# Performance work log

Hardware: AMD Instinct MI355X
Metric: run time of the kernel (lower is better)

## Reference

```python
import jax, jax.numpy as jnp
import numpy as np

N_HEAD = 16  # matches init_kwargs


def _rope_cos_sin(T, head_dim):
    # inv_freq over even indices, as in AdvancedRotaryEmbedding
    inv_freq = 1.0 / (10000.0 ** (jnp.arange(0, head_dim, 2, dtype=jnp.float32) / head_dim))
    t = jnp.arange(T, dtype=jnp.float32)
    freqs = t[:, None] * inv_freq[None, :]  # [T, head_dim/2]
    return jnp.cos(freqs), jnp.sin(freqs)


def _apply_rope(x, cos, sin):
    # x: [B, H, T, D]; cos/sin: [T, D/2] (broadcast over B, H)
    x1, x2 = x[..., 0::2], x[..., 1::2]
    # half-concat layout, faithful to the module's apply_rotary_emb
    return jnp.concatenate([x1 * cos - x2 * sin, x1 * sin + x2 * cos], axis=-1)


def reference(x, Wq, Wk, Wv, Wo):
    B, T, C = x.shape
    H = N_HEAD
    D = C // H
    # QKV projections (torch Linear: y = x @ W.T), then split heads -> [B, H, T, D]
    q = (x @ Wq.T).reshape(B, T, H, D).transpose(0, 2, 1, 3)
    k = (x @ Wk.T).reshape(B, T, H, D).transpose(0, 2, 1, 3)
    v = (x @ Wv.T).reshape(B, T, H, D).transpose(0, 2, 1, 3)
    cos, sin = _rope_cos_sin(T, D)
    cos = cos.astype(x.dtype)
    sin = sin.astype(x.dtype)
    q = _apply_rope(q, cos, sin)
    k = _apply_rope(k, cos, sin)
    # causal SDPA (eval mode -> dropout_p = 0); jax.nn expects [B, T, H, D]
    y = jax.nn.dot_product_attention(
        q.transpose(0, 2, 1, 3),
        k.transpose(0, 2, 1, 3),
        v.transpose(0, 2, 1, 3),
        is_causal=True,
    )  # [B, T, H, D]
    y = y.reshape(B, T, C)
    return y @ Wo.T


def setup_inputs() -> dict:
    key = jax.random.key(0)
    ks = jax.random.split(key, 5)
    B, T, C = 2, 2048, 1024
    s = 1.0 / np.sqrt(C)
    return {
        "x": jax.random.normal(ks[0], (B, T, C), dtype=jnp.float32),
        "Wq": jax.random.normal(ks[1], (C, C), dtype=jnp.float32) * s,
        "Wk": jax.random.normal(ks[2], (C, C), dtype=jnp.float32) * s,
        "Wv": jax.random.normal(ks[3], (C, C), dtype=jnp.float32) * s,
        "Wo": jax.random.normal(ks[4], (C, C), dtype=jnp.float32) * s,
    }
```

## Files before the change

### kernel.cpp

```cpp
#include <hip/hip_runtime.h>
#include <cstdint>
#include <cstddef>

typedef short s16x8 __attribute__((ext_vector_type(8)));
typedef float f32x4 __attribute__((ext_vector_type(4)));

#define MFMA16(a, b, c) __builtin_amdgcn_mfma_f32_16x16x32_bf16((a), (b), (c), 0, 0, 0)

constexpr int LDP = 72;

__device__ __forceinline__ short f2bf(float f) {
    unsigned u = __builtin_bit_cast(unsigned, f);
    u += 0x7FFFu + ((u >> 16) & 1u);
    return (short)(u >> 16);
}
__device__ __forceinline__ float bf2f(short s) {
    unsigned u = ((unsigned)(unsigned short)s) << 16;
    return __builtin_bit_cast(float, u);
}
__device__ __forceinline__ unsigned pack2(float a, float b) {
    return (unsigned)(unsigned short)f2bf(a) | ((unsigned)(unsigned short)f2bf(b) << 16);
}
__device__ __forceinline__ unsigned pack2t(float a, float b) {
    unsigned ua = __builtin_bit_cast(unsigned, a);
    unsigned ub = __builtin_bit_cast(unsigned, b);
    return (ua >> 16) | (ub & 0xFFFF0000u);
}

__device__ __forceinline__ void async_ld16(const void* g, void* l) {
    __builtin_amdgcn_global_load_lds(
        (const __attribute__((address_space(1))) unsigned int*)g,
        (__attribute__((address_space(3))) unsigned int*)l, 16, 0, 0);
}

__global__ __launch_bounds__(256) void convert_kernel(
    const float* __restrict__ x, const float* __restrict__ Wq,
    const float* __restrict__ Wk, const float* __restrict__ Wv,
    const float* __restrict__ Wo, short* __restrict__ xb, short* __restrict__ wb) {
    const size_t f = ((size_t)blockIdx.x * 256 + threadIdx.x) * 8;
    const float* src;
    short* dst;
    if (f < 4194304) { src = x + f; dst = xb + f; }
    else {
        size_t wo = f - 4194304;
        int seg = (int)(wo >> 20);
        const float* ws4[4] = {Wq, Wk, Wv, Wo};
        src = ws4[seg] + (wo & 1048575u);
        dst = wb + wo;
    }
    float4 a = ((const float4*)src)[0];
    float4 b = ((const float4*)src)[1];
    *(uint4*)dst = make_uint4(pack2(a.x, a.y), pack2(a.z, a.w),
                              pack2(b.x, b.y), pack2(b.z, b.w));
}

__global__ __launch_bounds__(256) void qkv_kernel(
    const short* __restrict__ xb, const short* __restrict__ wb,
    short* __restrict__ Qo, short* __restrict__ Ko, short* __restrict__ VTo) {
    __shared__ __align__(16) short sA[128 * 64];
    __shared__ __align__(16) short sB[128 * 64];
    const int tid = threadIdx.x;
    const int w = tid >> 6, lane = tid & 63, quad = lane >> 4, l15 = lane & 15;
    const int wm = w & 1, wn = w >> 1;
    const int bx = blockIdx.x, by = blockIdx.y;
    const int m0 = by * 128;
    const int nb = bx * 128;

    f32x4 acc[4][4];
#pragma unroll
    for (int i = 0; i < 4; i++)
#pragma unroll
        for (int j = 0; j < 4; j++) acc[i][j] = f32x4{0.f, 0.f, 0.f, 0.f};

    for (int kb = 0; kb < 16; kb++) {
        const int k0 = kb * 64;
        if (kb) __syncthreads();
#pragma unroll
        for (int i = 0; i < 4; i++) {
            int c = i * 256 + tid;
            int row = c >> 3, col8 = (c & 7) * 8;
            async_ld16(xb + (size_t)(m0 + row) * 1024 + k0 + col8,
                       &sA[(i * 256 + w * 64) * 8]);
            async_ld16(wb + (size_t)(nb + row) * 1024 + k0 + col8,
                       &sB[(i * 256 + w * 64) * 8]);
        }
        __syncthreads();
#pragma unroll
        for (int ks = 0; ks < 2; ks++) {
            s16x8 av[4], bv[4];
#pragma unroll
            for (int at = 0; at < 4; at++)
                av[at] = *(const s16x8*)&sA[(wm * 64 + at * 16 + l15) * 64 + ks * 32 + quad * 8];
#pragma unroll
            for (int bt = 0; bt < 4; bt++)
                bv[bt] = *(const s16x8*)&sB[(wn * 64 + bt * 16 + l15) * 64 + ks * 32 + quad * 8];
#pragma unroll
            for (int at = 0; at < 4; at++)
#pragma unroll
                for (int bt = 0; bt < 4; bt++)
                    acc[at][bt] = MFMA16(av[at], bv[bt], acc[at][bt]);
        }
    }

    const int wsel = bx >> 3;
    const int h = (bx & 7) * 2 + wn;
    if (wsel == 2) {
#pragma unroll
        for (int at = 0; at < 4; at++) {
            int m = m0 + wm * 64 + at * 16 + quad * 4;
            int b = m >> 11, t0 = m & 2047;
            size_t base = ((size_t)((b * 16 + h) * 64)) * 2048;
#pragma unroll
            for (int bt = 0; bt < 4; bt++) {
                int d = bt * 16 + l15;
                unsigned lo = pack2(acc[at][bt][0], acc[at][bt][1]);
                unsigned hi = pack2(acc[at][bt][2], acc[at][bt][3]);
                *(uint2*)&VTo[base + (size_t)d * 2048 + t0] = make_uint2(lo, hi);
            }
        }
    } else {
        short* Out = (wsel == 0) ? Qo : Ko;
#pragma unroll
        for (int at = 0; at < 4; at++)
#pragma unroll
            for (int r = 0; r < 4; r++) {
                int m = m0 + wm * 64 + at * 16 + quad * 4 + r;
                int b = m >> 11, t = m & 2047;
                size_t base = (((size_t)(b * 16 + h)) * 2048 + t) * 64;
#pragma unroll
                for (int bt = 0; bt < 4; bt++)
                    Out[base + bt * 16 + l15] = f2bf(acc[at][bt][r]);
            }
    }
}

__global__ __launch_bounds__(256) void rope_kernel(short* __restrict__ Q, short* __restrict__ K) {
    const int rid = blockIdx.x * 256 + threadIdx.x;
    const bool isK = (rid & 65536) != 0;
    short* buf = isK ? K : Q;
    const float sc = isK ? 1.0f : 0.18033688011112042f;
    const int r2 = rid & 65535;
    const int t = r2 & 2047;
    short* row = buf + (size_t)r2 * 64;

    unsigned wv[32];
    const uint4* rp = (const uint4*)row;
#pragma unroll
    for (int c = 0; c < 8; c++) {
        uint4 v = rp[c];
        wv[c * 4 + 0] = v.x; wv[c * 4 + 1] = v.y; wv[c * 4 + 2] = v.z; wv[c * 4 + 3] = v.w;
    }
    float y1[32], y2[32];
    const float tf = (float)t;
#pragma unroll
    for (int i = 0; i < 32; i++) {
        float x1 = bf2f((short)(wv[i] & 0xFFFFu));
        float x2 = bf2f((short)(wv[i] >> 16));
        float inv = expf(-9.2103403719761836f * (float)i * (1.0f / 32.0f));
        float fr = tf * inv;
        float sn, cs;
        sincosf(fr, &sn, &cs);
        y1[i] = (x1 * cs - x2 * sn) * sc;
        y2[i] = (x1 * sn + x2 * cs) * sc;
    }
    unsigned ow[32];
#pragma unroll
    for (int i = 0; i < 16; i++) ow[i] = pack2(y1[2 * i], y1[2 * i + 1]);
#pragma unroll
    for (int i = 0; i < 16; i++) ow[16 + i] = pack2(y2[2 * i], y2[2 * i + 1]);
    uint4* wp = (uint4*)row;
#pragma unroll
    for (int c = 0; c < 8; c++)
        wp[c] = make_uint4(ow[c * 4 + 0], ow[c * 4 + 1], ow[c * 4 + 2], ow[c * 4 + 3]);
}

__global__ __launch_bounds__(256) void attn_kernel(
    const short* __restrict__ Q, const short* __restrict__ K,
    const short* __restrict__ VT, short* __restrict__ paO, float* __restrict__ ml) {
    __shared__ __align__(16) short sQP[64 * LDP];
    __shared__ __align__(16) short sK[64 * LDP];
    __shared__ __align__(16) short sVT[64 * LDP];

    const int tid = threadIdx.x;
    const int w = tid >> 6, lane = tid & 63, quad = lane >> 4, l15 = lane & 15;
    const int u = 79 - blockIdx.x;
    const int bh = blockIdx.y;

    int qt, c;
    if (u < 8)       { qt = u; c = 0; }
    else if (u < 24) { int v = u - 8;  qt = 8 + (v >> 1); c = v & 1; }
    else if (u < 48) { int v = u - 24; qt = 16 + v / 3;   c = v - 3 * (qt - 16); }
    else             { int v = u - 48; qt = 24 + (v >> 2); c = v & 3; }
    const int kt0 = c * 8;
    const int kt1 = min(kt0 + 7, qt);

    const short* Qp = Q + (size_t)bh * 2048 * 64;
    const short* Kp = K + (size_t)bh * 2048 * 64;
    const short* Vp = VT + (size_t)bh * 64 * 2048;

#pragma unroll
    for (int i = 0; i < 2; i++) {
        int p = tid + i * 256;
        int row = p >> 3, c8 = p & 7;
        uint4 v = *(const uint4*)(Qp + (size_t)(qt * 64 + row) * 64 + c8 * 8);
        *(uint4*)&sQP[row * LDP + c8 * 8] = v;
    }
    __syncthreads();
    s16x8 aq[2];
#pragma unroll
    for (int ks = 0; ks < 2; ks++)
        aq[ks] = *(const s16x8*)&sQP[(w * 16 + l15) * LDP + ks * 32 + quad * 8];

    f32x4 o[4];
#pragma unroll
    for (int i = 0; i < 4; i++) o[i] = f32x4{0.f, 0.f, 0.f, 0.f};
    float mrun = -INFINITY;
    float lrun = 0.f;
    const int q_idx = qt * 64 + w * 16 + l15;

    for (int kt = kt0; kt <= kt1; kt++) {
        __syncthreads();
#pragma unroll
        for (int i = 0; i < 2; i++) {
            int p = tid + i * 256;
            int row = p >> 3, c8 = p & 7;
            uint4 kv = *(const uint4*)(Kp + (size_t)(kt * 64 + row) * 64 + c8 * 8);
            *(uint4*)&sK[row * LDP + c8 * 8] = kv;
            uint4 vv = *(const uint4*)(Vp + (size_t)row * 2048 + kt * 64 + c8 * 8);
            *(uint4*)&sVT[row * LDP + c8 * 8] = vv;
        }
        __syncthreads();

        f32x4 sa[4];
#pragma unroll
        for (int i = 0; i < 4; i++) sa[i] = f32x4{0.f, 0.f, 0.f, 0.f};
#pragma unroll
        for (int ks = 0; ks < 2; ks++) {
#pragma unroll
            for (int ct = 0; ct < 4; ct++) {
                s16x8 kf = *(const s16x8*)&sK[(ct * 16 + l15) * LDP + ks * 32 + quad * 8];
                sa[ct] = MFMA16(kf, aq[ks], sa[ct]);
            }
        }

        const bool diag = (kt == qt);
        float ps[4][4];
#pragma unroll
        for (int ct = 0; ct < 4; ct++) {
            int kbase = kt * 64 + ct * 16 + quad * 4;
#pragma unroll
            for (int r = 0; r < 4; r++) {
                float s = sa[ct][r];
                if (diag && (kbase + r) > q_idx) s = -INFINITY;
                ps[ct][r] = s;
            }
        }
        float cm[4];
#pragma unroll
        for (int ct = 0; ct < 4; ct++)
            cm[ct] = fmaxf(fmaxf(ps[ct][0], ps[ct][1]), fmaxf(ps[ct][2], ps[ct][3]));
        float mx = fmaxf(fmaxf(cm[0], cm[1]), fmaxf(cm[2], cm[3]));
        mx = fmaxf(mx, __shfl_xor(mx, 16));
        mx = fmaxf(mx, __shfl_xor(mx, 32));
        float mnew = fmaxf(mrun, mx);
        float alpha = exp2f(mrun - mnew);
        mrun = mnew;
        float cs[4];
#pragma unroll
        for (int ct = 0; ct < 4; ct++) {
#pragma unroll
            for (int r = 0; r < 4; r++) ps[ct][r] = exp2f(ps[ct][r] - mnew);
            cs[ct] = (ps[ct][0] + ps[ct][1]) + (ps[ct][2] + ps[ct][3]);
        }
        float psum = (cs[0] + cs[1]) + (cs[2] + cs[3]);
        psum += __shfl_xor(psum, 16);
        psum += __shfl_xor(psum, 32);
        lrun = lrun * alpha + psum;

        float arow[4];
#pragma unroll
        for (int r = 0; r < 4; r++) arow[r] = __shfl(alpha, quad * 4 + r);
#pragma unroll
        for (int ct = 0; ct < 4; ct++)
#pragma unroll
            for (int r = 0; r < 4; r++) o[ct][r] *= arow[r];

#pragma unroll
        for (int ct = 0; ct < 4; ct++) {
            unsigned lo = pack2t(ps[ct][0], ps[ct][1]);
            unsigned hi = pack2t(ps[ct][2], ps[ct][3]);
            *(uint2*)&sQP[(w * 16 + l15) * LDP + ct * 16 + quad * 4] = make_uint2(lo, hi);
        }

#pragma unroll
        for (int ks2 = 0; ks2 < 2; ks2++) {
            s16x8 pa = *(const s16x8*)&sQP[(w * 16 + l15) * LDP + ks2 * 32 + quad * 8];
#pragma unroll
            for (int ct = 0; ct < 4; ct++) {
                s16x8 vb = *(const s16x8*)&sVT[(ct * 16 + l15) * LDP + ks2 * 32 + quad * 8];
                o[ct] = MFMA16(pa, vb, o[ct]);
            }
        }
    }

    const size_t pbase = ((size_t)(bh * 80 + u)) * 4096;
#pragma unroll
    for (int r = 0; r < 4; r++) {
        int row = w * 16 + quad * 4 + r;
#pragma unroll
        for (int ct = 0; ct < 4; ct++)
            paO[pbase + row * 64 + ct * 16 + l15] = f2bf(o[ct][r]);
    }
    if (quad == 0) {
        int mlbase = (bh * 80 + u) * 128;
        ml[mlbase + w * 16 + l15] = mrun;
        ml[mlbase + 64 + w * 16 + l15] = lrun;
    }
}

__global__ __launch_bounds__(256) void combine_kernel(
    const short* __restrict__ paO, const float* __restrict__ ml, short* __restrict__ Y) {
    const int qt = blockIdx.x, bh = blockIdx.y;
    const int b = bh >> 4, h = bh & 15;
    const int nch = (qt >> 3) + 1;
    int base;
    if (qt < 8) base = qt;
    else if (qt < 16) base = 8 + 2 * (qt - 8);
    else if (qt < 24) base = 24 + 3 * (qt - 16);
    else base = 48 + 4 * (qt - 24);

    const int row = threadIdx.x >> 2;
    const int cq = (threadIdx.x & 3) * 16;

    float mi[4], li[4];
    float M = -INFINITY;
    for (int i = 0; i < nch; i++) {
        int mlbase = (bh * 80 + base + i) * 128;
        mi[i] = ml[mlbase + row];
        li[i] = ml[mlbase + 64 + row];
        M = fmaxf(M, mi[i]);
    }
    float L = 0.f, ai[4];
    for (int i = 0; i < nch; i++) {
        ai[i] = exp2f(mi[i] - M);
        L += li[i] * ai[i];
    }
    const float inv = 1.0f / L;

    float acc[16];
#pragma unroll
    for (int j = 0; j < 16; j++) acc[j] = 0.f;
    for (int i = 0; i < nch; i++) {
        const short* p = paO + ((size_t)(bh * 80 + base + i)) * 4096 + row * 64 + cq;
        uint4 v0 = ((const uint4*)p)[0];
        uint4 v1 = ((const uint4*)p)[1];
        unsigned vs[8] = {v0.x, v0.y, v0.z, v0.w, v1.x, v1.y, v1.z, v1.w};
#pragma unroll
        for (int j = 0; j < 8; j++) {
            acc[2 * j + 0] += bf2f((short)(vs[j] & 0xFFFFu)) * ai[i];
            acc[2 * j + 1] += bf2f((short)(vs[j] >> 16)) * ai[i];
        }
    }
    const int t = qt * 64 + row;
    short* yp = Y + ((size_t)(b * 2048 + t)) * 1024 + h * 64 + cq;
    unsigned ow[8];
#pragma unroll
    for (int j = 0; j < 8; j++) ow[j] = pack2(acc[2 * j] * inv, acc[2 * j + 1] * inv);
    ((uint4*)yp)[0] = make_uint4(ow[0], ow[1], ow[2], ow[3]);
    ((uint4*)yp)[1] = make_uint4(ow[4], ow[5], ow[6], ow[7]);
}

__global__ __launch_bounds__(256) void oproj_kernel(
    const short* __restrict__ Yb, const short* __restrict__ Wob, float* __restrict__ out) {
    __shared__ __align__(16) short sA[128 * 64];
    __shared__ __align__(16) short sB[128 * 64];
    const int tid = threadIdx.x;
    const int w = tid >> 6, lane = tid & 63, quad = lane >> 4, l15 = lane & 15;
    const int wm = w & 1, wn = w >> 1;
    const int m0 = blockIdx.y * 128;
    const int nb = blockIdx.x * 128;

    f32x4 acc[4][4];
#pragma unroll
    for (int i = 0; i < 4; i++)
#pragma unroll
        for (int j = 0; j < 4; j++) acc[i][j] = f32x4{0.f, 0.f, 0.f, 0.f};

    for (int kb = 0; kb < 16; kb++) {
        const int k0 = kb * 64;
        if (kb) __syncthreads();
#pragma unroll
        for (int i = 0; i < 4; i++) {
            int c = i * 256 + tid;
            int row = c >> 3, col8 = (c & 7) * 8;
            async_ld16(Yb + (size_t)(m0 + row) * 1024 + k0 + col8,
                       &sA[(i * 256 + w * 64) * 8]);
            async_ld16(Wob + (size_t)(nb + row) * 1024 + k0 + col8,
                       &sB[(i * 256 + w * 64) * 8]);
        }
        __syncthreads();
#pragma unroll
        for (int ks = 0; ks < 2; ks++) {
            s16x8 av[4], bv[4];
#pragma unroll
            for (int at = 0; at < 4; at++)
                av[at] = *(const s16x8*)&sA[(wm * 64 + at * 16 + l15) * 64 + ks * 32 + quad * 8];
#pragma unroll
            for (int bt = 0; bt < 4; bt++)
                bv[bt] = *(const s16x8*)&sB[(wn * 64 + bt * 16 + l15) * 64 + ks * 32 + quad * 8];
#pragma unroll
            for (int at = 0; at < 4; at++)
#pragma unroll
                for (int bt = 0; bt < 4; bt++)
                    acc[at][bt] = MFMA16(av[at], bv[bt], acc[at][bt]);
        }
    }
#pragma unroll
    for (int at = 0; at < 4; at++)
#pragma unroll
        for (int r = 0; r < 4; r++) {
            int m = m0 + wm * 64 + at * 16 + quad * 4 + r;
#pragma unroll
            for (int bt = 0; bt < 4; bt++) {
                int n = nb + wn * 64 + bt * 16 + l15;
                out[(size_t)m * 1024 + n] = acc[at][bt][r];
            }
        }
}

extern "C" void kernel_launch(void* const* d_in, const int* in_sizes, int n_in,
                              void* d_out, int out_size, void* d_ws, size_t ws_size,
                              hipStream_t stream) {
    (void)in_sizes; (void)n_in; (void)out_size; (void)ws_size;
    const float* x  = (const float*)d_in[0];
    const float* Wq = (const float*)d_in[1];
    const float* Wk = (const float*)d_in[2];
    const float* Wv = (const float*)d_in[3];
    const float* Wo = (const float*)d_in[4];
    float* out = (float*)d_out;

    const size_t NE = (size_t)2 * 16 * 2048 * 64;
    short* Q   = (short*)d_ws;
    short* K   = Q + NE;
    short* VT  = K + NE;
    short* Y   = VT + NE;
    short* xb  = Y;
    short* wb  = Y + NE;
    short* paO = wb + NE;
    float* ml  = (float*)(paO + (size_t)32 * 80 * 4096);

    convert_kernel<<<4096, 256, 0, stream>>>(x, Wq, Wk, Wv, Wo, xb, wb);
    qkv_kernel<<<dim3(24, 32), 256, 0, stream>>>(xb, wb, Q, K, VT);
    rope_kernel<<<512, 256, 0, stream>>>(Q, K);
    attn_kernel<<<dim3(80, 32), 256, 0, stream>>>(Q, K, VT, paO, ml);
    combine_kernel<<<dim3(32, 32), 256, 0, stream>>>(paO, ml, Y);
    oproj_kernel<<<dim3(8, 32), 256, 0, stream>>>(Y, wb + 3 * 1048576, out);
}
```

Measured before the change: 217.7 us.

## Prefetch K/V tiles in registers, use hardware sincos, shrink oproj tiles

The attention kernel now loads the next K/V tile into registers while the current tile is being computed, which overlaps global latency with MFMA work. The causal mask is applied only on the diagonal tile. The RoPE kernel replaces expf/sincosf with exp2f and the hardware sin/cos builtins on a range-reduced argument, which may cost some accuracy. The output projection uses 64x128 tiles instead of 128x128, doubling the grid to 512 blocks to fill more CUs on the MI355X.

```diff
diff --git a/kernel.cpp b/kernel.cpp
--- a/kernel.cpp
+++ b/kernel.cpp
@@ -156,10 +156,11 @@
     for (int i = 0; i < 32; i++) {
         float x1 = bf2f((short)(wv[i] & 0xFFFFu));
         float x2 = bf2f((short)(wv[i] >> 16));
-        float inv = expf(-9.2103403719761836f * (float)i * (1.0f / 32.0f));
-        float fr = tf * inv;
-        float sn, cs;
-        sincosf(fr, &sn, &cs);
+        float inv = exp2f((float)i * -0.4152410118609203f);
+        float rev = tf * inv * 0.15915494309189535f;
+        rev = rev - floorf(rev);
+        float sn = __builtin_amdgcn_sinf(rev);
+        float cs = __builtin_amdgcn_cosf(rev);
         y1[i] = (x1 * cs - x2 * sn) * sc;
         y2[i] = (x1 * sn + x2 * cs) * sc;
     }
@@ -198,6 +199,13 @@
     const short* Kp = K + (size_t)bh * 2048 * 64;
     const short* Vp = VT + (size_t)bh * 64 * 2048;
 
+    const int ro = tid >> 3, co = (tid & 7) * 8;
+
+    uint4 rK0 = *(const uint4*)(Kp + (size_t)(kt0 * 64 + ro) * 64 + co);
+    uint4 rK1 = *(const uint4*)(Kp + (size_t)(kt0 * 64 + ro + 32) * 64 + co);
+    uint4 rV0 = *(const uint4*)(Vp + (size_t)ro * 2048 + kt0 * 64 + co);
+    uint4 rV1 = *(const uint4*)(Vp + (size_t)(ro + 32) * 2048 + kt0 * 64 + co);
+
 #pragma unroll
     for (int i = 0; i < 2; i++) {
         int p = tid + i * 256;
@@ -220,15 +228,15 @@
 
     for (int kt = kt0; kt <= kt1; kt++) {
         __syncthreads();
-#pragma unroll
-        for (int i = 0; i < 2; i++) {
-            int p = tid + i * 256;
-            int row = p >> 3, c8 = p & 7;
-            uint4 kv = *(const uint4*)(Kp + (size_t)(kt * 64 + row) * 64 + c8 * 8);
-            *(uint4*)&sK[row * LDP + c8 * 8] = kv;
-            uint4 vv = *(const uint4*)(Vp + (size_t)row * 2048 + kt * 64 + c8 * 8);
-            *(uint4*)&sVT[row * LDP + c8 * 8] = vv;
-        }
+        *(uint4*)&sK[ro * LDP + co] = rK0;
+        *(uint4*)&sK[(ro + 32) * LDP + co] = rK1;
+        *(uint4*)&sVT[ro * LDP + co] = rV0;
+        *(uint4*)&sVT[(ro + 32) * LDP + co] = rV1;
+        const int ktn = (kt < kt1) ? kt + 1 : kt;
+        rK0 = *(const uint4*)(Kp + (size_t)(ktn * 64 + ro) * 64 + co);
+        rK1 = *(const uint4*)(Kp + (size_t)(ktn * 64 + ro + 32) * 64 + co);
+        rV0 = *(const uint4*)(Vp + (size_t)ro * 2048 + ktn * 64 + co);
+        rV1 = *(const uint4*)(Vp + (size_t)(ro + 32) * 2048 + ktn * 64 + co);
         __syncthreads();
 
         f32x4 sa[4];
@@ -243,18 +251,22 @@
             }
         }
 
-        const bool diag = (kt == qt);
         float ps[4][4];
 #pragma unroll
-        for (int ct = 0; ct < 4; ct++) {
-            int kbase = kt * 64 + ct * 16 + quad * 4;
-#pragma unroll
-            for (int r = 0; r < 4; r++) {
-                float s = sa[ct][r];
-                if (diag && (kbase + r) > q_idx) s = -INFINITY;
-                ps[ct][r] = s;
-            }
-        }
+        for (int ct = 0; ct < 4; ct++)
+#pragma unroll
+            for (int r = 0; r < 4; r++) ps[ct][r] = sa[ct][r];
+
+        if (kt == qt) {
+#pragma unroll
+            for (int ct = 0; ct < 4; ct++) {
+                int kbase = kt * 64 + ct * 16 + quad * 4;
+#pragma unroll
+                for (int r = 0; r < 4; r++)
+                    if ((kbase + r) > q_idx) ps[ct][r] = -INFINITY;
+            }
+        }
+
         float cm[4];
 #pragma unroll
         for (int ct = 0; ct < 4; ct++)
@@ -372,46 +384,50 @@
 
 __global__ __launch_bounds__(256) void oproj_kernel(
     const short* __restrict__ Yb, const short* __restrict__ Wob, float* __restrict__ out) {
-    __shared__ __align__(16) short sA[128 * 64];
+    __shared__ __align__(16) short sA[64 * 64];
     __shared__ __align__(16) short sB[128 * 64];
     const int tid = threadIdx.x;
     const int w = tid >> 6, lane = tid & 63, quad = lane >> 4, l15 = lane & 15;
-    const int wm = w & 1, wn = w >> 1;
-    const int m0 = blockIdx.y * 128;
+    const int m0 = blockIdx.y * 64;
     const int nb = blockIdx.x * 128;
 
-    f32x4 acc[4][4];
+    f32x4 acc[4][2];
 #pragma unroll
     for (int i = 0; i < 4; i++)
 #pragma unroll
-        for (int j = 0; j < 4; j++) acc[i][j] = f32x4{0.f, 0.f, 0.f, 0.f};
+        for (int j = 0; j < 2; j++) acc[i][j] = f32x4{0.f, 0.f, 0.f, 0.f};
 
     for (int kb = 0; kb < 16; kb++) {
         const int k0 = kb * 64;
         if (kb) __syncthreads();
 #pragma unroll
-        for (int i = 0; i < 4; i++) {
+        for (int i = 0; i < 2; i++) {
             int c = i * 256 + tid;
             int row = c >> 3, col8 = (c & 7) * 8;
             async_ld16(Yb + (size_t)(m0 + row) * 1024 + k0 + col8,
                        &sA[(i * 256 + w * 64) * 8]);
+        }
+#pragma unroll
+        for (int i = 0; i < 4; i++) {
+            int c = i * 256 + tid;
+            int row = c >> 3, col8 = (c & 7) * 8;
             async_ld16(Wob + (size_t)(nb + row) * 1024 + k0 + col8,
                        &sB[(i * 256 + w * 64) * 8]);
         }
         __syncthreads();
 #pragma unroll
         for (int ks = 0; ks < 2; ks++) {
-            s16x8 av[4], bv[4];
+            s16x8 av[4], bv[2];
 #pragma unroll
             for (int at = 0; at < 4; at++)
-                av[at] = *(const s16x8*)&sA[(wm * 64 + at * 16 + l15) * 64 + ks * 32 + quad * 8];
-#pragma unroll
-            for (int bt = 0; bt < 4; bt++)
-                bv[bt] = *(const s16x8*)&sB[(wn * 64 + bt * 16 + l15) * 64 + ks * 32 + quad * 8];
+                av[at] = *(const s16x8*)&sA[(at * 16 + l15) * 64 + ks * 32 + quad * 8];
+#pragma unroll
+            for (int bt = 0; bt < 2; bt++)
+                bv[bt] = *(const s16x8*)&sB[(w * 32 + bt * 16 + l15) * 64 + ks * 32 + quad * 8];
 #pragma unroll
             for (int at = 0; at < 4; at++)
 #pragma unroll
-                for (int bt = 0; bt < 4; bt++)
+                for (int bt = 0; bt < 2; bt++)
                     acc[at][bt] = MFMA16(av[at], bv[bt], acc[at][bt]);
         }
     }
@@ -419,10 +435,10 @@
     for (int at = 0; at < 4; at++)
 #pragma unroll
         for (int r = 0; r < 4; r++) {
-            int m = m0 + wm * 64 + at * 16 + quad * 4 + r;
-#pragma unroll
-            for (int bt = 0; bt < 4; bt++) {
-                int n = nb + wn * 64 + bt * 16 + l15;
+            int m = m0 + at * 16 + quad * 4 + r;
+#pragma unroll
+            for (int bt = 0; bt < 2; bt++) {
+                int n = nb + w * 32 + bt * 16 + l15;
                 out[(size_t)m * 1024 + n] = acc[at][bt][r];
             }
         }
@@ -454,5 +470,5 @@
     rope_kernel<<<512, 256, 0, stream>>>(Q, K);
     attn_kernel<<<dim3(80, 32), 256, 0, stream>>>(Q, K, VT, paO, ml);
     combine_kernel<<<dim3(32, 32), 256, 0, stream>>>(paO, ml, Y);
-    oproj_kernel<<<dim3(8, 32), 256, 0, stream>>>(Y, wb + 3 * 1048576, out);
-}
+    oproj_kernel<<<dim3(8, 64), 256, 0, stream>>>(Y, wb + 3 * 1048576, out);
+}
```

After: 211.7 us. -2.7%, faster.
